# Performance work log

Hardware: AMD Instinct MI355X
Metric: run time of the kernel (lower is better)

The kernel has to match this reference:

```python
import jax, jax.numpy as jnp
import numpy as np

B_SZ, L, D, N = 4, 2048, 768, 16


def setup_inputs() -> dict:
    key = jax.random.key(0)
    ks = jax.random.split(key, 8)
    x = jax.random.normal(ks[0], (B_SZ, L, D), dtype=jnp.float32)
    # A_log initialized as log(arange(1..N)) repeated over d, as in the module
    A_log = jnp.log(jnp.broadcast_to(jnp.arange(1, N + 1, dtype=jnp.float32), (D, N)))
    # s_b_c: Linear(D, 2N)
    W_bc = jax.random.normal(ks[1], (2 * N, D), dtype=jnp.float32) / jnp.sqrt(D)
    b_bc = jnp.zeros((2 * N,), dtype=jnp.float32)
    # s_1: Linear(D, 1)
    W_1 = jax.random.normal(ks[2], (1, D), dtype=jnp.float32) / jnp.sqrt(D)
    b_1 = jnp.zeros((1,), dtype=jnp.float32)
    # s_delta: Linear(1, D)
    W_d = jax.random.normal(ks[3], (D, 1), dtype=jnp.float32)
    b_d = jnp.zeros((D,), dtype=jnp.float32)
    return {"x": x, "A_log": A_log, "W_bc": W_bc, "b_bc": b_bc,
            "W_1": W_1, "b_1": b_1, "W_d": W_d, "b_d": b_d}


def reference(x, A_log, W_bc, b_bc, W_1, b_1, W_d, b_d):
    b, l, d = x.shape
    n = A_log.shape[1]
    A = -jnp.exp(A_log)                                   # (d, n)
    BandC = x @ W_bc.T + b_bc                             # (b, l, 2n)
    Bm, Cm = BandC[..., :n], BandC[..., n:]               # (b, l, n) each
    # delta = softplus(s_delta(s_1(x)))  -> (b, l, d)
    s1 = x @ W_1.T + b_1                                  # (b, l, 1)
    delta = jax.nn.softplus(s1 @ W_d.T + b_d)             # (b, l, d)
    deltaA = jnp.exp(jnp.einsum('bld,dn->bldn', delta, A))        # (b, l, d, n)
    deltaB_u = jnp.einsum('bld,bln,bld->bldn', delta, Bm, x)      # (b, l, d, n)

    # sequential selective-scan over time with lax.scan
    dA_t = jnp.moveaxis(deltaA, 1, 0)      # (l, b, d, n)
    dBu_t = jnp.moveaxis(deltaB_u, 1, 0)   # (l, b, d, n)
    C_t = jnp.moveaxis(Cm, 1, 0)           # (l, b, n)

    def step(h, inp):
        dA_i, dBu_i, c_i = inp
        h = dA_i * h + dBu_i               # (b, d, n)
        y = jnp.einsum('bdn,bn->bd', h, c_i)
        return h, y

    h0 = jnp.zeros((b, d, n), dtype=x.dtype)
    _, ys = jax.lax.scan(step, h0, (dA_t, dBu_t, C_t))
    return jnp.moveaxis(ys, 0, 1)          # (b, l, d)
```

## Files before the change

kernel.cpp:

```cpp
#include <hip/hip_runtime.h>

#define L_SEQ 2048
#define D_DIM 768
#define N_ST 16
#define NB 4
#define NJ 33
#define NROWS (NB * L_SEQ)
#define PROJ_ELEMS (NROWS * NJ)

#define DSPLIT 8
#define DSEG (D_DIM / DSPLIT)
#define DK 32
#define NCHUNK (DSEG / DK)
#define RB 128
#define XST 132
#define WST 64

__device__ __forceinline__ float fast_exp2(float x) {
#if __has_builtin(__builtin_amdgcn_exp2f)
  return __builtin_amdgcn_exp2f(x);
#else
  return __expf(x * 0.69314718055994531f);
#endif
}

__device__ __forceinline__ float softplus_f(float v) {
  float e = fast_exp2(v * 1.44269504088896f);
  float l = __log2f(1.0f + e) * 0.69314718055994531f;
  return (v > 15.0f) ? v : l;
}

__device__ __forceinline__ void pow_tree(float e1, float pw[N_ST]) {
  pw[0] = e1;
  pw[1] = pw[0] * pw[0];
  pw[2] = pw[1] * pw[0];
  pw[3] = pw[1] * pw[1];
  pw[4] = pw[3] * pw[0];
  pw[5] = pw[3] * pw[1];
  pw[6] = pw[3] * pw[2];
  pw[7] = pw[3] * pw[3];
  pw[8] = pw[7] * pw[0];
  pw[9] = pw[7] * pw[1];
  pw[10] = pw[7] * pw[2];
  pw[11] = pw[7] * pw[3];
  pw[12] = pw[7] * pw[4];
  pw[13] = pw[7] * pw[5];
  pw[14] = pw[7] * pw[6];
  pw[15] = pw[7] * pw[7];
}

__global__ __launch_bounds__(256) void k_proj_gemm(
    const float* __restrict__ x, const float* __restrict__ W_bc,
    const float* __restrict__ W_1, float* __restrict__ PBC) {
  __shared__ float xs_t[DK * XST];
  __shared__ float ws_t[DK * WST];

  const int ds  = blockIdx.x % DSPLIT;
  const int rb0 = (blockIdx.x / DSPLIT) * RB;
  const int dbase = ds * DSEG;
  const int tid = threadIdx.x;

  const int rg = tid & 31;
  const int jg = tid >> 5;

  float acc[4][5];
#pragma unroll
  for (int i = 0; i < 4; ++i)
#pragma unroll
    for (int k = 0; k < 5; ++k) acc[i][k] = 0.0f;

  const int lrow = tid >> 1;
  const int lhalf = (tid & 1) * 16;
  const float* xg_row = x + (size_t)(rb0 + lrow) * D_DIM + dbase + lhalf;

  for (int ch = 0; ch < NCHUNK; ++ch) {
    const int dc = dbase + ch * DK;
    float4 xv[4];
#pragma unroll
    for (int q = 0; q < 4; ++q)
      xv[q] = *(const float4*)(xg_row + ch * DK + q * 4);
    float wv[8];
    int widx[8];
#pragma unroll
    for (int u = 0; u < 8; ++u) {
      int idx = tid + u * 256;
      int dk = idx >> 6, slot = idx & 63;
      int wjg = slot >> 3, wk = slot & 7;
      int j = wjg + 8 * wk;
      float v = 0.0f;
      if (wk < 5) {
        if (j < 32)       v = W_bc[(size_t)j * D_DIM + dc + dk];
        else if (j == 32) v = W_1[dc + dk];
      }
      wv[u] = v; widx[u] = dk * WST + slot;
    }
    __syncthreads();
#pragma unroll
    for (int q = 0; q < 4; ++q) {
      xs_t[(lhalf + q * 4 + 0) * XST + lrow] = xv[q].x;
      xs_t[(lhalf + q * 4 + 1) * XST + lrow] = xv[q].y;
      xs_t[(lhalf + q * 4 + 2) * XST + lrow] = xv[q].z;
      xs_t[(lhalf + q * 4 + 3) * XST + lrow] = xv[q].w;
    }
#pragma unroll
    for (int u = 0; u < 8; ++u) ws_t[widx[u]] = wv[u];
    __syncthreads();
#pragma unroll 8
    for (int dk = 0; dk < DK; ++dk) {
      float4 xr = *(const float4*)&xs_t[dk * XST + rg * 4];
      float4 wr = *(const float4*)&ws_t[dk * WST + jg * 8];
      float w4  = ws_t[dk * WST + jg * 8 + 4];
      float xa[4] = {xr.x, xr.y, xr.z, xr.w};
      float wa[5] = {wr.x, wr.y, wr.z, wr.w, w4};
#pragma unroll
      for (int i = 0; i < 4; ++i)
#pragma unroll
        for (int k = 0; k < 5; ++k)
          acc[i][k] = fmaf(xa[i], wa[k], acc[i][k]);
    }
  }

  float* pb = PBC + (size_t)ds * PROJ_ELEMS;
#pragma unroll
  for (int i = 0; i < 4; ++i) {
    int row = rb0 + rg * 4 + i;
#pragma unroll
    for (int k = 0; k < 5; ++k) {
      int j = jg + 8 * k;
      if (k < 4 || jg == 0) pb[(size_t)row * NJ + j] = acc[i][k];
    }
  }
}

__global__ __launch_bounds__(256) void k_proj_reduce(
    const float* __restrict__ PBC, const float* __restrict__ b_bc,
    const float* __restrict__ b_1, float* __restrict__ BC33) {
  const int idx = blockIdx.x * 256 + threadIdx.x;
  const int j = idx % NJ;
  float s = 0.0f;
#pragma unroll
  for (int k = 0; k < DSPLIT; ++k) s += PBC[(size_t)k * PROJ_ELEMS + idx];
  s += (j < 32) ? b_bc[j] : b_1[0];
  BC33[idx] = s;
}

template <int LC>
__global__ __launch_bounds__(256) void k_scan1(
    const float* __restrict__ x, const float* __restrict__ A_log,
    const float* __restrict__ W_d, const float* __restrict__ b_d,
    const float* __restrict__ BC33, float* __restrict__ DS,
    float* __restrict__ H, int NC) {
  const int cb = blockIdx.x % 3;
  const int c  = (blockIdx.x / 3) % NC;
  const int b  = blockIdx.x / (3 * NC);
  const int d  = cb * 256 + threadIdx.x;

  const float wd = W_d[d], bd = b_d[d];
  float Aln[N_ST];
  {
    const float4* al4 = (const float4*)(A_log + (size_t)d * N_ST);
#pragma unroll
    for (int q = 0; q < 4; ++q) {
      float4 v = al4[q];
      Aln[4*q+0] = -__expf(v.x) * 1.44269504088896f;
      Aln[4*q+1] = -__expf(v.y) * 1.44269504088896f;
      Aln[4*q+2] = -__expf(v.z) * 1.44269504088896f;
      Aln[4*q+3] = -__expf(v.w) * 1.44269504088896f;
    }
  }

  bool geom = true;
#pragma unroll
  for (int n = 1; n < N_ST; ++n) {
    float ref = (float)(n + 1) * Aln[0];
    geom = geom && (fabsf(Aln[n] - ref) <= 1e-4f * fabsf(ref) + 1e-12f);
  }
  const float a0 = Aln[0];

  float h[N_ST];
#pragma unroll
  for (int n = 0; n < N_ST; ++n) h[n] = 0.0f;
  float dsum = 0.0f;

  const int l0 = c * LC;
  const float* bc = BC33 + (size_t)(b * L_SEQ + l0) * NJ;
  const float* xp = x + (size_t)(b * L_SEQ + l0) * D_DIM + d;

  if (geom) {
#pragma unroll 8
    for (int l = 0; l < LC; ++l) {
      float s1 = bc[l * NJ + 32];
      float delta = softplus_f(fmaf(s1, wd, bd));
      float xv = xp[(size_t)l * D_DIM];
      float f = delta * xv;
      dsum += delta;
      float pw[N_ST];
      pow_tree(fast_exp2(a0 * delta), pw);
#pragma unroll
      for (int n = 0; n < N_ST; ++n)
        h[n] = fmaf(pw[n], h[n], f * bc[l * NJ + n]);
    }
  } else {
#pragma unroll 4
    for (int l = 0; l < LC; ++l) {
      float s1 = bc[l * NJ + 32];
      float delta = softplus_f(fmaf(s1, wd, bd));
      float xv = xp[(size_t)l * D_DIM];
      float f = delta * xv;
      dsum += delta;
#pragma unroll
      for (int n = 0; n < N_ST; ++n) {
        float dA = fast_exp2(delta * Aln[n]);
        h[n] = fmaf(dA, h[n], f * bc[l * NJ + n]);
      }
    }
  }

  DS[((size_t)b * NC + c) * D_DIM + d] = dsum;
  size_t base = ((size_t)(b * NC + c) * D_DIM + d) * N_ST;
  float4* H4 = (float4*)(H + base);
#pragma unroll
  for (int q = 0; q < 4; ++q)
    H4[q] = make_float4(h[4*q], h[4*q+1], h[4*q+2], h[4*q+3]);
}

__global__ __launch_bounds__(256) void k_combine(
    const float* __restrict__ A_log, const float* __restrict__ DS,
    float* __restrict__ H, int NC) {
  const int b  = blockIdx.x / 48;
  const int tl = (blockIdx.x % 48) * 256 + threadIdx.x;
  const int d = tl >> 4, n = tl & 15;
  const float Aln = -__expf(A_log[d * N_ST + n]) * 1.44269504088896f;

  const float* dsp = DS + (size_t)b * NC * D_DIM + d;
  float* Hp = H + (size_t)b * NC * (D_DIM * N_ST) + tl;

  float h = 0.0f;
  float ds_c = dsp[0];
  float hold = Hp[0];
#pragma unroll 8
  for (int c = 0; c < NC; ++c) {
    float ds_n = 0.0f, hold_n = 0.0f;
    if (c + 1 < NC) {
      ds_n   = dsp[(size_t)(c + 1) * D_DIM];
      hold_n = Hp[(size_t)(c + 1) * (D_DIM * N_ST)];
    }
    float p = fast_exp2(Aln * ds_c);
    Hp[(size_t)c * (D_DIM * N_ST)] = h;
    h = fmaf(p, h, hold);
    ds_c = ds_n; hold = hold_n;
  }
}

template <int LC>
__global__ __launch_bounds__(256) void k_scan2(
    const float* __restrict__ x, const float* __restrict__ A_log,
    const float* __restrict__ W_d, const float* __restrict__ b_d,
    const float* __restrict__ BC33, const float* __restrict__ HIN,
    float* __restrict__ out, int NC) {
  const int cb = blockIdx.x % 3;
  const int c  = (blockIdx.x / 3) % NC;
  const int b  = blockIdx.x / (3 * NC);
  const int d  = cb * 256 + threadIdx.x;

  const float wd = W_d[d], bd = b_d[d];
  float Aln[N_ST];
  {
    const float4* al4 = (const float4*)(A_log + (size_t)d * N_ST);
#pragma unroll
    for (int q = 0; q < 4; ++q) {
      float4 v = al4[q];
      Aln[4*q+0] = -__expf(v.x) * 1.44269504088896f;
      Aln[4*q+1] = -__expf(v.y) * 1.44269504088896f;
      Aln[4*q+2] = -__expf(v.z) * 1.44269504088896f;
      Aln[4*q+3] = -__expf(v.w) * 1.44269504088896f;
    }
  }

  bool geom = true;
#pragma unroll
  for (int n = 1; n < N_ST; ++n) {
    float ref = (float)(n + 1) * Aln[0];
    geom = geom && (fabsf(Aln[n] - ref) <= 1e-4f * fabsf(ref) + 1e-12f);
  }
  const float a0 = Aln[0];

  float h[N_ST];
  size_t base = ((size_t)(b * NC + c) * D_DIM + d) * N_ST;
  const float4* HIN4 = (const float4*)(HIN + base);
#pragma unroll
  for (int q = 0; q < 4; ++q) {
    float4 v = HIN4[q];
    h[4*q] = v.x; h[4*q+1] = v.y; h[4*q+2] = v.z; h[4*q+3] = v.w;
  }

  const int l0 = c * LC;
  const float* bc = BC33 + (size_t)(b * L_SEQ + l0) * NJ;
  const float* xp = x + (size_t)(b * L_SEQ + l0) * D_DIM + d;
  float* op = out + (size_t)(b * L_SEQ + l0) * D_DIM + d;

  if (geom) {
#pragma unroll 8
    for (int l = 0; l < LC; ++l) {
      float s1 = bc[l * NJ + 32];
      float delta = softplus_f(fmaf(s1, wd, bd));
      float xv = xp[(size_t)l * D_DIM];
      float f = delta * xv;
      float pw[N_ST];
      pow_tree(fast_exp2(a0 * delta), pw);
      float y = 0.0f;
#pragma unroll
      for (int n = 0; n < N_ST; ++n) {
        h[n] = fmaf(pw[n], h[n], f * bc[l * NJ + n]);
        y = fmaf(h[n], bc[l * NJ + 16 + n], y);
      }
      op[(size_t)l * D_DIM] = y;
    }
  } else {
#pragma unroll 4
    for (int l = 0; l < LC; ++l) {
      float s1 = bc[l * NJ + 32];
      float delta = softplus_f(fmaf(s1, wd, bd));
      float xv = xp[(size_t)l * D_DIM];
      float f = delta * xv;
      float y = 0.0f;
#pragma unroll
      for (int n = 0; n < N_ST; ++n) {
        float dA = fast_exp2(delta * Aln[n]);
        h[n] = fmaf(dA, h[n], f * bc[l * NJ + n]);
        y = fmaf(h[n], bc[l * NJ + 16 + n], y);
      }
      op[(size_t)l * D_DIM] = y;
    }
  }
}

extern "C" void kernel_launch(void* const* d_in, const int* in_sizes, int n_in,
                              void* d_out, int out_size, void* d_ws, size_t ws_size,
                              hipStream_t stream) {
  const float* x     = (const float*)d_in[0];
  const float* A_log = (const float*)d_in[1];
  const float* W_bc  = (const float*)d_in[2];
  const float* b_bc  = (const float*)d_in[3];
  const float* W_1   = (const float*)d_in[4];
  const float* b_1   = (const float*)d_in[5];
  const float* W_d   = (const float*)d_in[6];
  const float* b_d   = (const float*)d_in[7];
  float* out = (float*)d_out;
  float* ws  = (float*)d_ws;

  int NC = 8;
  const int cands[4] = {64, 32, 16, 8};
  for (int i = 0; i < 4; ++i) {
    size_t need = (9ull * PROJ_ELEMS + (3072ull + 49152ull) * cands[i]) * 4ull;
    if (ws_size >= need) { NC = cands[i]; break; }
  }

  float* BC33 = ws;
  float* PBC  = ws + PROJ_ELEMS;
  float* DSb  = PBC + (size_t)DSPLIT * PROJ_ELEMS;
  float* H    = DSb + (size_t)3072 * NC;

  k_proj_gemm<<<(NROWS / RB) * DSPLIT, 256, 0, stream>>>(x, W_bc, W_1, PBC);
  k_proj_reduce<<<PROJ_ELEMS / 256, 256, 0, stream>>>(PBC, b_bc, b_1, BC33);

  const int gs = 3 * NB * NC;
  switch (NC) {
    case 64:
      k_scan1<32><<<gs, 256, 0, stream>>>(x, A_log, W_d, b_d, BC33, DSb, H, NC);
      k_combine<<<192, 256, 0, stream>>>(A_log, DSb, H, NC);
      k_scan2<32><<<gs, 256, 0, stream>>>(x, A_log, W_d, b_d, BC33, H, out, NC);
      break;
    case 32:
      k_scan1<64><<<gs, 256, 0, stream>>>(x, A_log, W_d, b_d, BC33, DSb, H, NC);
      k_combine<<<192, 256, 0, stream>>>(A_log, DSb, H, NC);
      k_scan2<64><<<gs, 256, 0, stream>>>(x, A_log, W_d, b_d, BC33, H, out, NC);
      break;
    case 16:
      k_scan1<128><<<gs, 256, 0, stream>>>(x, A_log, W_d, b_d, BC33, DSb, H, NC);
      k_combine<<<192, 256, 0, stream>>>(A_log, DSb, H, NC);
      k_scan2<128><<<gs, 256, 0, stream>>>(x, A_log, W_d, b_d, BC33, H, out, NC);
      break;
    default:
      k_scan1<256><<<gs, 256, 0, stream>>>(x, A_log, W_d, b_d, BC33, DSb, H, NC);
      k_combine<<<192, 256, 0, stream>>>(A_log, DSb, H, NC);
      k_scan2<256><<<gs, 256, 0, stream>>>(x, A_log, W_d, b_d, BC33, H, out, NC);
      break;
  }
}
```

Before: 170.4 us.

## Fuse chunked scan phases into one cooperative kernel with cached local outputs

Replaces the three scan kernels (chunk scan, cross-chunk combine, rescan) with one cooperative kernel that uses grid syncs between phases. The first pass keeps the zero-initial-state outputs in LDS. The second pass no longer reruns the recurrence; it adds a correction term built from the carried-in state, the cumulative delta decay and C. Packed float2 math is used for the geometric power tree. This removes two launches and the redundant recurrence and x reads, at the cost of 32KB LDS per block, grid-wide barriers and a co-residency requirement for 768 blocks, with a fallback path if the cooperative launch fails.

New measurement: 359.5 us. 111% more time.

```diff
diff --git a/kernel.cpp b/kernel.cpp
--- a/kernel.cpp
+++ b/kernel.cpp
@@ -1,4 +1,7 @@
 #include <hip/hip_runtime.h>
+#include <hip/hip_cooperative_groups.h>
+
+namespace cg = cooperative_groups;
 
 #define L_SEQ 2048
 #define D_DIM 768
@@ -7,6 +10,7 @@
 #define NJ 33
 #define NROWS (NB * L_SEQ)
 #define PROJ_ELEMS (NROWS * NJ)
+#define DN (D_DIM * N_ST)
 
 #define DSPLIT 8
 #define DSEG (D_DIM / DSPLIT)
@@ -16,6 +20,8 @@
 #define XST 132
 #define WST 64
 
+typedef float v2f __attribute__((ext_vector_type(2)));
+
 __device__ __forceinline__ float fast_exp2(float x) {
 #if __has_builtin(__builtin_amdgcn_exp2f)
   return __builtin_amdgcn_exp2f(x);
@@ -30,23 +36,26 @@
   return (v > 15.0f) ? v : l;
 }
 
+__device__ __forceinline__ void pow_tree2(float e1, v2f pw2[8]) {
+  float e2s = e1 * e1;
+  float e4s = e2s * e2s;
+  float e8s = e4s * e4s;
+  v2f s2 = {e2s, e2s}, s4 = {e4s, e4s}, s8 = {e8s, e8s};
+  pw2[0] = (v2f){e1, e2s};
+  pw2[1] = pw2[0] * s2;
+  pw2[2] = pw2[0] * s4;
+  pw2[3] = pw2[1] * s4;
+  pw2[4] = pw2[0] * s8;
+  pw2[5] = pw2[1] * s8;
+  pw2[6] = pw2[2] * s8;
+  pw2[7] = pw2[3] * s8;
+}
+
 __device__ __forceinline__ void pow_tree(float e1, float pw[N_ST]) {
-  pw[0] = e1;
-  pw[1] = pw[0] * pw[0];
-  pw[2] = pw[1] * pw[0];
-  pw[3] = pw[1] * pw[1];
-  pw[4] = pw[3] * pw[0];
-  pw[5] = pw[3] * pw[1];
-  pw[6] = pw[3] * pw[2];
-  pw[7] = pw[3] * pw[3];
-  pw[8] = pw[7] * pw[0];
-  pw[9] = pw[7] * pw[1];
-  pw[10] = pw[7] * pw[2];
-  pw[11] = pw[7] * pw[3];
-  pw[12] = pw[7] * pw[4];
-  pw[13] = pw[7] * pw[5];
-  pw[14] = pw[7] * pw[6];
-  pw[15] = pw[7] * pw[7];
+  pw[0] = e1;  pw[1] = pw[0]*pw[0];  pw[2] = pw[1]*pw[0];  pw[3] = pw[1]*pw[1];
+  pw[4] = pw[3]*pw[0]; pw[5] = pw[3]*pw[1]; pw[6] = pw[3]*pw[2]; pw[7] = pw[3]*pw[3];
+  pw[8] = pw[7]*pw[0]; pw[9] = pw[7]*pw[1]; pw[10]= pw[7]*pw[2]; pw[11]= pw[7]*pw[3];
+  pw[12]= pw[7]*pw[4]; pw[13]= pw[7]*pw[5]; pw[14]= pw[7]*pw[6]; pw[15]= pw[7]*pw[7];
 }
 
 __global__ __launch_bounds__(256) void k_proj_gemm(
@@ -59,7 +68,6 @@
   const int rb0 = (blockIdx.x / DSPLIT) * RB;
   const int dbase = ds * DSEG;
   const int tid = threadIdx.x;
-
   const int rg = tid & 31;
   const int jg = tid >> 5;
 
@@ -142,6 +150,197 @@
   for (int k = 0; k < DSPLIT; ++k) s += PBC[(size_t)k * PROJ_ELEMS + idx];
   s += (j < 32) ? b_bc[j] : b_1[0];
   BC33[idx] = s;
+}
+
+template <int LC>
+__global__ __launch_bounds__(256) void k_scan_coop(
+    const float* __restrict__ x, const float* __restrict__ A_log,
+    const float* __restrict__ W_d, const float* __restrict__ b_d,
+    const float* __restrict__ BC33, float* __restrict__ DS,
+    float* __restrict__ H, float* __restrict__ out) {
+  constexpr int NC = L_SEQ / LC;
+  __shared__ float ylds[LC * 256];
+  const int tid = threadIdx.x;
+  const int bid = blockIdx.x;
+  const int cb = bid % 3;
+  const int c  = (bid / 3) % NC;
+  const int b  = bid / (3 * NC);
+  const int d  = cb * 256 + tid;
+
+  const float wd = W_d[d], bd = b_d[d];
+  float Aln[N_ST];
+  {
+    const float4* al4 = (const float4*)(A_log + (size_t)d * N_ST);
+#pragma unroll
+    for (int q = 0; q < 4; ++q) {
+      float4 v = al4[q];
+      Aln[4*q+0] = -__expf(v.x) * 1.44269504088896f;
+      Aln[4*q+1] = -__expf(v.y) * 1.44269504088896f;
+      Aln[4*q+2] = -__expf(v.z) * 1.44269504088896f;
+      Aln[4*q+3] = -__expf(v.w) * 1.44269504088896f;
+    }
+  }
+  bool geom = true;
+#pragma unroll
+  for (int n = 1; n < N_ST; ++n) {
+    float ref = (float)(n + 1) * Aln[0];
+    geom = geom && (fabsf(Aln[n] - ref) <= 1e-4f * fabsf(ref) + 1e-12f);
+  }
+  const float a0 = Aln[0];
+
+  const int l0 = c * LC;
+  const float* bc = BC33 + (size_t)(b * L_SEQ + l0) * NJ;
+  const float* xp = x + (size_t)(b * L_SEQ + l0) * D_DIM + d;
+
+  v2f h2[8];
+#pragma unroll
+  for (int k = 0; k < 8; ++k) h2[k] = (v2f){0.0f, 0.0f};
+  float dsum = 0.0f;
+
+  if (geom) {
+#pragma unroll 8
+    for (int l = 0; l < LC; ++l) {
+      float s1 = bc[l * NJ + 32];
+      float delta = softplus_f(fmaf(s1, wd, bd));
+      float xv = xp[(size_t)l * D_DIM];
+      float f = delta * xv;
+      dsum += delta;
+      v2f pw2[8];
+      pow_tree2(fast_exp2(a0 * delta), pw2);
+      v2f f2 = {f, f};
+      v2f y2 = {0.0f, 0.0f};
+#pragma unroll
+      for (int k = 0; k < 8; ++k) {
+        v2f B2 = {bc[l * NJ + 2*k], bc[l * NJ + 2*k + 1]};
+        v2f C2 = {bc[l * NJ + 16 + 2*k], bc[l * NJ + 16 + 2*k + 1]};
+        h2[k] = pw2[k] * h2[k] + f2 * B2;
+        y2 = y2 + h2[k] * C2;
+      }
+      ylds[l * 256 + tid] = y2.x + y2.y;
+    }
+  } else {
+#pragma unroll 4
+    for (int l = 0; l < LC; ++l) {
+      float s1 = bc[l * NJ + 32];
+      float delta = softplus_f(fmaf(s1, wd, bd));
+      float xv = xp[(size_t)l * D_DIM];
+      float f = delta * xv;
+      dsum += delta;
+      float y = 0.0f;
+#pragma unroll
+      for (int k = 0; k < 8; ++k) {
+        float dA0 = fast_exp2(delta * Aln[2*k]);
+        float dA1 = fast_exp2(delta * Aln[2*k+1]);
+        h2[k].x = fmaf(dA0, h2[k].x, f * bc[l * NJ + 2*k]);
+        h2[k].y = fmaf(dA1, h2[k].y, f * bc[l * NJ + 2*k + 1]);
+        y = fmaf(h2[k].x, bc[l * NJ + 16 + 2*k], y);
+        y = fmaf(h2[k].y, bc[l * NJ + 16 + 2*k + 1], y);
+      }
+      ylds[l * 256 + tid] = y;
+    }
+  }
+
+  DS[((size_t)b * NC + c) * D_DIM + d] = dsum;
+  {
+    size_t base = ((size_t)(b * NC + c) * D_DIM + d) * N_ST;
+    float4* H4 = (float4*)(H + base);
+#pragma unroll
+    for (int q = 0; q < 4; ++q)
+      H4[q] = make_float4(h2[2*q].x, h2[2*q].y, h2[2*q+1].x, h2[2*q+1].y);
+  }
+
+  cg::this_grid().sync();
+
+  if (bid < 192) {
+    const int bb = bid / 48;
+    const int tl = (bid % 48) * 256 + tid;
+    const int dd = tl >> 4, nn = tl & 15;
+    const float Aln1 = -__expf(A_log[dd * N_ST + nn]) * 1.44269504088896f;
+    const float* dsp = DS + (size_t)bb * NC * D_DIM + dd;
+    float* Hp = H + (size_t)bb * NC * DN + tl;
+
+    float h = 0.0f;
+    float pds[8], ph[8];
+#pragma unroll
+    for (int k = 0; k < 8; ++k) {
+      pds[k] = dsp[(size_t)k * D_DIM];
+      ph[k]  = Hp[(size_t)k * DN];
+    }
+    for (int g = 0; g < NC; g += 8) {
+      float nds[8], nh[8];
+      if (g + 8 < NC) {
+#pragma unroll
+        for (int k = 0; k < 8; ++k) {
+          nds[k] = dsp[(size_t)(g + 8 + k) * D_DIM];
+          nh[k]  = Hp[(size_t)(g + 8 + k) * DN];
+        }
+      }
+#pragma unroll
+      for (int k = 0; k < 8; ++k) {
+        float p = fast_exp2(Aln1 * pds[k]);
+        Hp[(size_t)(g + k) * DN] = h;
+        h = fmaf(p, h, ph[k]);
+      }
+#pragma unroll
+      for (int k = 0; k < 8; ++k) { pds[k] = nds[k]; ph[k] = nh[k]; }
+    }
+  }
+
+  cg::this_grid().sync();
+
+  float* op = out + (size_t)(b * L_SEQ + l0) * D_DIM + d;
+  if (c == 0) {
+#pragma unroll 8
+    for (int l = 0; l < LC; ++l)
+      op[(size_t)l * D_DIM] = ylds[l * 256 + tid];
+    return;
+  }
+
+  v2f hin2[8];
+  {
+    size_t base = ((size_t)(b * NC + c) * D_DIM + d) * N_ST;
+    const float4* HIN4 = (const float4*)(H + base);
+#pragma unroll
+    for (int q = 0; q < 4; ++q) {
+      float4 v = HIN4[q];
+      hin2[2*q]   = (v2f){v.x, v.y};
+      hin2[2*q+1] = (v2f){v.z, v.w};
+    }
+  }
+
+  if (geom) {
+    float S = 0.0f;
+#pragma unroll 8
+    for (int l = 0; l < LC; ++l) {
+      float s1 = bc[l * NJ + 32];
+      float delta = softplus_f(fmaf(s1, wd, bd));
+      S += delta;
+      v2f pw2[8];
+      pow_tree2(fast_exp2(a0 * S), pw2);
+      v2f acc = {0.0f, 0.0f};
+#pragma unroll
+      for (int k = 0; k < 8; ++k) {
+        v2f C2 = {bc[l * NJ + 16 + 2*k], bc[l * NJ + 16 + 2*k + 1]};
+        acc = acc + pw2[k] * (hin2[k] * C2);
+      }
+      op[(size_t)l * D_DIM] = ylds[l * 256 + tid] + acc.x + acc.y;
+    }
+  } else {
+    float S = 0.0f;
+#pragma unroll 4
+    for (int l = 0; l < LC; ++l) {
+      float s1 = bc[l * NJ + 32];
+      float delta = softplus_f(fmaf(s1, wd, bd));
+      S += delta;
+      float corr = 0.0f;
+#pragma unroll
+      for (int k = 0; k < 8; ++k) {
+        corr = fmaf(fast_exp2(Aln[2*k]   * S) * hin2[k].x, bc[l * NJ + 16 + 2*k],     corr);
+        corr = fmaf(fast_exp2(Aln[2*k+1] * S) * hin2[k].y, bc[l * NJ + 16 + 2*k + 1], corr);
+      }
+      op[(size_t)l * D_DIM] = ylds[l * 256 + tid] + corr;
+    }
+  }
 }
 
 template <int LC>
@@ -154,21 +353,11 @@
   const int c  = (blockIdx.x / 3) % NC;
   const int b  = blockIdx.x / (3 * NC);
   const int d  = cb * 256 + threadIdx.x;
-
   const float wd = W_d[d], bd = b_d[d];
   float Aln[N_ST];
-  {
-    const float4* al4 = (const float4*)(A_log + (size_t)d * N_ST);
-#pragma unroll
-    for (int q = 0; q < 4; ++q) {
-      float4 v = al4[q];
-      Aln[4*q+0] = -__expf(v.x) * 1.44269504088896f;
-      Aln[4*q+1] = -__expf(v.y) * 1.44269504088896f;
-      Aln[4*q+2] = -__expf(v.z) * 1.44269504088896f;
-      Aln[4*q+3] = -__expf(v.w) * 1.44269504088896f;
-    }
-  }
-
+#pragma unroll
+  for (int n = 0; n < N_ST; ++n)
+    Aln[n] = -__expf(A_log[d * N_ST + n]) * 1.44269504088896f;
   bool geom = true;
 #pragma unroll
   for (int n = 1; n < N_ST; ++n) {
@@ -176,23 +365,19 @@
     geom = geom && (fabsf(Aln[n] - ref) <= 1e-4f * fabsf(ref) + 1e-12f);
   }
   const float a0 = Aln[0];
-
   float h[N_ST];
 #pragma unroll
   for (int n = 0; n < N_ST; ++n) h[n] = 0.0f;
   float dsum = 0.0f;
-
   const int l0 = c * LC;
   const float* bc = BC33 + (size_t)(b * L_SEQ + l0) * NJ;
   const float* xp = x + (size_t)(b * L_SEQ + l0) * D_DIM + d;
-
   if (geom) {
 #pragma unroll 8
     for (int l = 0; l < LC; ++l) {
       float s1 = bc[l * NJ + 32];
       float delta = softplus_f(fmaf(s1, wd, bd));
-      float xv = xp[(size_t)l * D_DIM];
-      float f = delta * xv;
+      float f = delta * xp[(size_t)l * D_DIM];
       dsum += delta;
       float pw[N_ST];
       pow_tree(fast_exp2(a0 * delta), pw);
@@ -205,17 +390,13 @@
     for (int l = 0; l < LC; ++l) {
       float s1 = bc[l * NJ + 32];
       float delta = softplus_f(fmaf(s1, wd, bd));
-      float xv = xp[(size_t)l * D_DIM];
-      float f = delta * xv;
+      float f = delta * xp[(size_t)l * D_DIM];
       dsum += delta;
 #pragma unroll
-      for (int n = 0; n < N_ST; ++n) {
-        float dA = fast_exp2(delta * Aln[n]);
-        h[n] = fmaf(dA, h[n], f * bc[l * NJ + n]);
-      }
-    }
-  }
-
+      for (int n = 0; n < N_ST; ++n)
+        h[n] = fmaf(fast_exp2(delta * Aln[n]), h[n], f * bc[l * NJ + n]);
+    }
+  }
   DS[((size_t)b * NC + c) * D_DIM + d] = dsum;
   size_t base = ((size_t)(b * NC + c) * D_DIM + d) * N_ST;
   float4* H4 = (float4*)(H + base);
@@ -231,10 +412,8 @@
   const int tl = (blockIdx.x % 48) * 256 + threadIdx.x;
   const int d = tl >> 4, n = tl & 15;
   const float Aln = -__expf(A_log[d * N_ST + n]) * 1.44269504088896f;
-
   const float* dsp = DS + (size_t)b * NC * D_DIM + d;
-  float* Hp = H + (size_t)b * NC * (D_DIM * N_ST) + tl;
-
+  float* Hp = H + (size_t)b * NC * DN + tl;
   float h = 0.0f;
   float ds_c = dsp[0];
   float hold = Hp[0];
@@ -243,10 +422,10 @@
     float ds_n = 0.0f, hold_n = 0.0f;
     if (c + 1 < NC) {
       ds_n   = dsp[(size_t)(c + 1) * D_DIM];
-      hold_n = Hp[(size_t)(c + 1) * (D_DIM * N_ST)];
+      hold_n = Hp[(size_t)(c + 1) * DN];
     }
     float p = fast_exp2(Aln * ds_c);
-    Hp[(size_t)c * (D_DIM * N_ST)] = h;
+    Hp[(size_t)c * DN] = h;
     h = fmaf(p, h, hold);
     ds_c = ds_n; hold = hold_n;
   }
@@ -262,21 +441,11 @@
   const int c  = (blockIdx.x / 3) % NC;
   const int b  = blockIdx.x / (3 * NC);
   const int d  = cb * 256 + threadIdx.x;
-
   const float wd = W_d[d], bd = b_d[d];
   float Aln[N_ST];
-  {
-    const float4* al4 = (const float4*)(A_log + (size_t)d * N_ST);
-#pragma unroll
-    for (int q = 0; q < 4; ++q) {
-      float4 v = al4[q];
-      Aln[4*q+0] = -__expf(v.x) * 1.44269504088896f;
-      Aln[4*q+1] = -__expf(v.y) * 1.44269504088896f;
-      Aln[4*q+2] = -__expf(v.z) * 1.44269504088896f;
-      Aln[4*q+3] = -__expf(v.w) * 1.44269504088896f;
-    }
-  }
-
+#pragma unroll
+  for (int n = 0; n < N_ST; ++n)
+    Aln[n] = -__expf(A_log[d * N_ST + n]) * 1.44269504088896f;
   bool geom = true;
 #pragma unroll
   for (int n = 1; n < N_ST; ++n) {
@@ -284,7 +453,6 @@
     geom = geom && (fabsf(Aln[n] - ref) <= 1e-4f * fabsf(ref) + 1e-12f);
   }
   const float a0 = Aln[0];
-
   float h[N_ST];
   size_t base = ((size_t)(b * NC + c) * D_DIM + d) * N_ST;
   const float4* HIN4 = (const float4*)(HIN + base);
@@ -293,19 +461,16 @@
     float4 v = HIN4[q];
     h[4*q] = v.x; h[4*q+1] = v.y; h[4*q+2] = v.z; h[4*q+3] = v.w;
   }
-
   const int l0 = c * LC;
   const float* bc = BC33 + (size_t)(b * L_SEQ + l0) * NJ;
   const float* xp = x + (size_t)(b * L_SEQ + l0) * D_DIM + d;
   float* op = out + (size_t)(b * L_SEQ + l0) * D_DIM + d;
-
   if (geom) {
 #pragma unroll 8
     for (int l = 0; l < LC; ++l) {
       float s1 = bc[l * NJ + 32];
       float delta = softplus_f(fmaf(s1, wd, bd));
-      float xv = xp[(size_t)l * D_DIM];
-      float f = delta * xv;
+      float f = delta * xp[(size_t)l * D_DIM];
       float pw[N_ST];
       pow_tree(fast_exp2(a0 * delta), pw);
       float y = 0.0f;
@@ -321,13 +486,11 @@
     for (int l = 0; l < LC; ++l) {
       float s1 = bc[l * NJ + 32];
       float delta = softplus_f(fmaf(s1, wd, bd));
-      float xv = xp[(size_t)l * D_DIM];
-      float f = delta * xv;
+      float f = delta * xp[(size_t)l * D_DIM];
       float y = 0.0f;
 #pragma unroll
       for (int n = 0; n < N_ST; ++n) {
-        float dA = fast_exp2(delta * Aln[n]);
-        h[n] = fmaf(dA, h[n], f * bc[l * NJ + n]);
+        h[n] = fmaf(fast_exp2(delta * Aln[n]), h[n], f * bc[l * NJ + n]);
         y = fmaf(h[n], bc[l * NJ + 16 + n], y);
       }
       op[(size_t)l * D_DIM] = y;
@@ -349,11 +512,10 @@
   float* out = (float*)d_out;
   float* ws  = (float*)d_ws;
 
-  int NC = 8;
-  const int cands[4] = {64, 32, 16, 8};
-  for (int i = 0; i < 4; ++i) {
-    size_t need = (9ull * PROJ_ELEMS + (3072ull + 49152ull) * cands[i]) * 4ull;
-    if (ws_size >= need) { NC = cands[i]; break; }
+  int NC = 64;
+  {
+    size_t need = (9ull * PROJ_ELEMS + (3072ull + 49152ull) * 64) * 4ull;
+    if (ws_size < need) NC = 32;
   }
 
   float* BC33 = ws;
@@ -365,26 +527,30 @@
   k_proj_reduce<<<PROJ_ELEMS / 256, 256, 0, stream>>>(PBC, b_bc, b_1, BC33);
 
   const int gs = 3 * NB * NC;
-  switch (NC) {
-    case 64:
+  const float* xa = x; const float* ala = A_log;
+  const float* wda = W_d; const float* bda = b_d;
+  const float* bca = BC33; float* dsa = DSb; float* ha = H; float* oa = out;
+  void* args[] = {(void*)&xa, (void*)&ala, (void*)&wda, (void*)&bda,
+                  (void*)&bca, (void*)&dsa, (void*)&ha, (void*)&oa};
+
+  hipError_t ce;
+  if (NC == 64) {
+    ce = hipLaunchCooperativeKernel(reinterpret_cast<void*>(&k_scan_coop<32>),
+                                    dim3(gs), dim3(256), args, 0, stream);
+  } else {
+    ce = hipLaunchCooperativeKernel(reinterpret_cast<void*>(&k_scan_coop<64>),
+                                    dim3(gs), dim3(256), args, 0, stream);
+  }
+  if (ce != hipSuccess) {
+    (void)hipGetLastError();
+    if (NC == 64) {
       k_scan1<32><<<gs, 256, 0, stream>>>(x, A_log, W_d, b_d, BC33, DSb, H, NC);
       k_combine<<<192, 256, 0, stream>>>(A_log, DSb, H, NC);
       k_scan2<32><<<gs, 256, 0, stream>>>(x, A_log, W_d, b_d, BC33, H, out, NC);
-      break;
-    case 32:
+    } else {
       k_scan1<64><<<gs, 256, 0, stream>>>(x, A_log, W_d, b_d, BC33, DSb, H, NC);
       k_combine<<<192, 256, 0, stream>>>(A_log, DSb, H, NC);
       k_scan2<64><<<gs, 256, 0, stream>>>(x, A_log, W_d, b_d, BC33, H, out, NC);
-      break;
-    case 16:
-      k_scan1<128><<<gs, 256, 0, stream>>>(x, A_log, W_d, b_d, BC33, DSb, H, NC);
-      k_combine<<<192, 256, 0, stream>>>(A_log, DSb, H, NC);
-      k_scan2<128><<<gs, 256, 0, stream>>>(x, A_log, W_d, b_d, BC33, H, out, NC);
-      break;
-    default:
-      k_scan1<256><<<gs, 256, 0, stream>>>(x, A_log, W_d, b_d, BC33, DSb, H, NC);
-      k_combine<<<192, 256, 0, stream>>>(A_log, DSb, H, NC);
-      k_scan2<256><<<gs, 256, 0, stream>>>(x, A_log, W_d, b_d, BC33, H, out, NC);
-      break;
-  }
-}
+    }
+  }
+}
```

## Pad BC rows to 48 floats, vectorize scan with packed float2 math, batch combine loads

Applied to the files above, without the earlier changes.

The projection reduce now writes B, C and s1 into rows padded to 48 floats, so the scan kernels can read B and C with aligned float4 loads instead of scalar loads at stride 33. The state recurrence and the output dot product are rewritten over two-wide float vectors, aiming at packed FP32 instructions, and the power tree is built the same way. The chunk-combine kernel loads eight chunks at a time to overlap memory latency. The padding enlarges the BC buffer, and the workspace sizing now falls back only to 32 chunks.

After: 151.9 us. 1.12x faster.

```diff
diff --git a/kernel.cpp b/kernel.cpp
--- a/kernel.cpp
+++ b/kernel.cpp
@@ -5,8 +5,10 @@
 #define N_ST 16
 #define NB 4
 #define NJ 33
+#define BCS 48
 #define NROWS (NB * L_SEQ)
 #define PROJ_ELEMS (NROWS * NJ)
+#define DN (D_DIM * N_ST)
 
 #define DSPLIT 8
 #define DSEG (D_DIM / DSPLIT)
@@ -16,6 +18,8 @@
 #define XST 132
 #define WST 64
 
+typedef float v2f __attribute__((ext_vector_type(2)));
+
 __device__ __forceinline__ float fast_exp2(float x) {
 #if __has_builtin(__builtin_amdgcn_exp2f)
   return __builtin_amdgcn_exp2f(x);
@@ -30,23 +34,19 @@
   return (v > 15.0f) ? v : l;
 }
 
-__device__ __forceinline__ void pow_tree(float e1, float pw[N_ST]) {
-  pw[0] = e1;
-  pw[1] = pw[0] * pw[0];
-  pw[2] = pw[1] * pw[0];
-  pw[3] = pw[1] * pw[1];
-  pw[4] = pw[3] * pw[0];
-  pw[5] = pw[3] * pw[1];
-  pw[6] = pw[3] * pw[2];
-  pw[7] = pw[3] * pw[3];
-  pw[8] = pw[7] * pw[0];
-  pw[9] = pw[7] * pw[1];
-  pw[10] = pw[7] * pw[2];
-  pw[11] = pw[7] * pw[3];
-  pw[12] = pw[7] * pw[4];
-  pw[13] = pw[7] * pw[5];
-  pw[14] = pw[7] * pw[6];
-  pw[15] = pw[7] * pw[7];
+__device__ __forceinline__ void pow_tree2(float e1, v2f pw2[8]) {
+  float e2s = e1 * e1;
+  float e4s = e2s * e2s;
+  float e8s = e4s * e4s;
+  v2f s2 = {e2s, e2s}, s4 = {e4s, e4s}, s8 = {e8s, e8s};
+  pw2[0] = (v2f){e1, e2s};
+  pw2[1] = pw2[0] * s2;
+  pw2[2] = pw2[0] * s4;
+  pw2[3] = pw2[1] * s4;
+  pw2[4] = pw2[0] * s8;
+  pw2[5] = pw2[1] * s8;
+  pw2[6] = pw2[2] * s8;
+  pw2[7] = pw2[3] * s8;
 }
 
 __global__ __launch_bounds__(256) void k_proj_gemm(
@@ -59,7 +59,6 @@
   const int rb0 = (blockIdx.x / DSPLIT) * RB;
   const int dbase = ds * DSEG;
   const int tid = threadIdx.x;
-
   const int rg = tid & 31;
   const int jg = tid >> 5;
 
@@ -134,21 +133,22 @@
 
 __global__ __launch_bounds__(256) void k_proj_reduce(
     const float* __restrict__ PBC, const float* __restrict__ b_bc,
-    const float* __restrict__ b_1, float* __restrict__ BC33) {
+    const float* __restrict__ b_1, float* __restrict__ BC48) {
   const int idx = blockIdx.x * 256 + threadIdx.x;
-  const int j = idx % NJ;
+  const int row = idx / NJ;
+  const int j = idx - row * NJ;
   float s = 0.0f;
 #pragma unroll
   for (int k = 0; k < DSPLIT; ++k) s += PBC[(size_t)k * PROJ_ELEMS + idx];
   s += (j < 32) ? b_bc[j] : b_1[0];
-  BC33[idx] = s;
+  BC48[(size_t)row * BCS + j] = s;
 }
 
 template <int LC>
 __global__ __launch_bounds__(256) void k_scan1(
     const float* __restrict__ x, const float* __restrict__ A_log,
     const float* __restrict__ W_d, const float* __restrict__ b_d,
-    const float* __restrict__ BC33, float* __restrict__ DS,
+    const float* __restrict__ BC48, float* __restrict__ DS,
     float* __restrict__ H, int NC) {
   const int cb = blockIdx.x % 3;
   const int c  = (blockIdx.x / 3) % NC;
@@ -168,7 +168,6 @@
       Aln[4*q+3] = -__expf(v.w) * 1.44269504088896f;
     }
   }
-
   bool geom = true;
 #pragma unroll
   for (int n = 1; n < N_ST; ++n) {
@@ -177,41 +176,52 @@
   }
   const float a0 = Aln[0];
 
-  float h[N_ST];
-#pragma unroll
-  for (int n = 0; n < N_ST; ++n) h[n] = 0.0f;
+  v2f h2[8];
+#pragma unroll
+  for (int k = 0; k < 8; ++k) h2[k] = (v2f){0.0f, 0.0f};
   float dsum = 0.0f;
 
   const int l0 = c * LC;
-  const float* bc = BC33 + (size_t)(b * L_SEQ + l0) * NJ;
+  const float* bc = BC48 + (size_t)(b * L_SEQ + l0) * BCS;
   const float* xp = x + (size_t)(b * L_SEQ + l0) * D_DIM + d;
 
   if (geom) {
 #pragma unroll 8
     for (int l = 0; l < LC; ++l) {
-      float s1 = bc[l * NJ + 32];
+      const float* r = bc + l * BCS;
+      float4 B0 = *(const float4*)(r + 0);
+      float4 B1 = *(const float4*)(r + 4);
+      float4 B2 = *(const float4*)(r + 8);
+      float4 B3 = *(const float4*)(r + 12);
+      float s1 = r[32];
       float delta = softplus_f(fmaf(s1, wd, bd));
       float xv = xp[(size_t)l * D_DIM];
       float f = delta * xv;
       dsum += delta;
-      float pw[N_ST];
-      pow_tree(fast_exp2(a0 * delta), pw);
-#pragma unroll
-      for (int n = 0; n < N_ST; ++n)
-        h[n] = fmaf(pw[n], h[n], f * bc[l * NJ + n]);
+      v2f pw2[8];
+      pow_tree2(fast_exp2(a0 * delta), pw2);
+      v2f f2 = {f, f};
+      h2[0] = pw2[0] * h2[0] + f2 * (v2f){B0.x, B0.y};
+      h2[1] = pw2[1] * h2[1] + f2 * (v2f){B0.z, B0.w};
+      h2[2] = pw2[2] * h2[2] + f2 * (v2f){B1.x, B1.y};
+      h2[3] = pw2[3] * h2[3] + f2 * (v2f){B1.z, B1.w};
+      h2[4] = pw2[4] * h2[4] + f2 * (v2f){B2.x, B2.y};
+      h2[5] = pw2[5] * h2[5] + f2 * (v2f){B2.z, B2.w};
+      h2[6] = pw2[6] * h2[6] + f2 * (v2f){B3.x, B3.y};
+      h2[7] = pw2[7] * h2[7] + f2 * (v2f){B3.z, B3.w};
     }
   } else {
 #pragma unroll 4
     for (int l = 0; l < LC; ++l) {
-      float s1 = bc[l * NJ + 32];
+      const float* r = bc + l * BCS;
+      float s1 = r[32];
       float delta = softplus_f(fmaf(s1, wd, bd));
-      float xv = xp[(size_t)l * D_DIM];
-      float f = delta * xv;
+      float f = delta * xp[(size_t)l * D_DIM];
       dsum += delta;
 #pragma unroll
-      for (int n = 0; n < N_ST; ++n) {
-        float dA = fast_exp2(delta * Aln[n]);
-        h[n] = fmaf(dA, h[n], f * bc[l * NJ + n]);
+      for (int k = 0; k < 8; ++k) {
+        h2[k].x = fmaf(fast_exp2(delta * Aln[2*k]),   h2[k].x, f * r[2*k]);
+        h2[k].y = fmaf(fast_exp2(delta * Aln[2*k+1]), h2[k].y, f * r[2*k+1]);
       }
     }
   }
@@ -221,7 +231,7 @@
   float4* H4 = (float4*)(H + base);
 #pragma unroll
   for (int q = 0; q < 4; ++q)
-    H4[q] = make_float4(h[4*q], h[4*q+1], h[4*q+2], h[4*q+3]);
+    H4[q] = make_float4(h2[2*q].x, h2[2*q].y, h2[2*q+1].x, h2[2*q+1].y);
 }
 
 __global__ __launch_bounds__(256) void k_combine(
@@ -230,25 +240,34 @@
   const int b  = blockIdx.x / 48;
   const int tl = (blockIdx.x % 48) * 256 + threadIdx.x;
   const int d = tl >> 4, n = tl & 15;
-  const float Aln = -__expf(A_log[d * N_ST + n]) * 1.44269504088896f;
-
+  const float Aln1 = -__expf(A_log[d * N_ST + n]) * 1.44269504088896f;
   const float* dsp = DS + (size_t)b * NC * D_DIM + d;
-  float* Hp = H + (size_t)b * NC * (D_DIM * N_ST) + tl;
+  float* Hp = H + (size_t)b * NC * DN + tl;
 
   float h = 0.0f;
-  float ds_c = dsp[0];
-  float hold = Hp[0];
-#pragma unroll 8
-  for (int c = 0; c < NC; ++c) {
-    float ds_n = 0.0f, hold_n = 0.0f;
-    if (c + 1 < NC) {
-      ds_n   = dsp[(size_t)(c + 1) * D_DIM];
-      hold_n = Hp[(size_t)(c + 1) * (D_DIM * N_ST)];
-    }
-    float p = fast_exp2(Aln * ds_c);
-    Hp[(size_t)c * (D_DIM * N_ST)] = h;
-    h = fmaf(p, h, hold);
-    ds_c = ds_n; hold = hold_n;
+  float pds[8], ph[8];
+#pragma unroll
+  for (int k = 0; k < 8; ++k) {
+    pds[k] = dsp[(size_t)k * D_DIM];
+    ph[k]  = Hp[(size_t)k * DN];
+  }
+  for (int g = 0; g < NC; g += 8) {
+    float nds[8], nh[8];
+    if (g + 8 < NC) {
+#pragma unroll
+      for (int k = 0; k < 8; ++k) {
+        nds[k] = dsp[(size_t)(g + 8 + k) * D_DIM];
+        nh[k]  = Hp[(size_t)(g + 8 + k) * DN];
+      }
+    }
+#pragma unroll
+    for (int k = 0; k < 8; ++k) {
+      float p = fast_exp2(Aln1 * pds[k]);
+      Hp[(size_t)(g + k) * DN] = h;
+      h = fmaf(p, h, ph[k]);
+    }
+#pragma unroll
+    for (int k = 0; k < 8; ++k) { pds[k] = nds[k]; ph[k] = nh[k]; }
   }
 }
 
@@ -256,7 +275,7 @@
 __global__ __launch_bounds__(256) void k_scan2(
     const float* __restrict__ x, const float* __restrict__ A_log,
     const float* __restrict__ W_d, const float* __restrict__ b_d,
-    const float* __restrict__ BC33, const float* __restrict__ HIN,
+    const float* __restrict__ BC48, const float* __restrict__ HIN,
     float* __restrict__ out, int NC) {
   const int cb = blockIdx.x % 3;
   const int c  = (blockIdx.x / 3) % NC;
@@ -276,7 +295,6 @@
       Aln[4*q+3] = -__expf(v.w) * 1.44269504088896f;
     }
   }
-
   bool geom = true;
 #pragma unroll
   for (int n = 1; n < N_ST; ++n) {
@@ -285,50 +303,67 @@
   }
   const float a0 = Aln[0];
 
-  float h[N_ST];
-  size_t base = ((size_t)(b * NC + c) * D_DIM + d) * N_ST;
-  const float4* HIN4 = (const float4*)(HIN + base);
-#pragma unroll
-  for (int q = 0; q < 4; ++q) {
-    float4 v = HIN4[q];
-    h[4*q] = v.x; h[4*q+1] = v.y; h[4*q+2] = v.z; h[4*q+3] = v.w;
+  v2f h2[8];
+  {
+    size_t base = ((size_t)(b * NC + c) * D_DIM + d) * N_ST;
+    const float4* HIN4 = (const float4*)(HIN + base);
+#pragma unroll
+    for (int q = 0; q < 4; ++q) {
+      float4 v = HIN4[q];
+      h2[2*q]   = (v2f){v.x, v.y};
+      h2[2*q+1] = (v2f){v.z, v.w};
+    }
   }
 
   const int l0 = c * LC;
-  const float* bc = BC33 + (size_t)(b * L_SEQ + l0) * NJ;
+  const float* bc = BC48 + (size_t)(b * L_SEQ + l0) * BCS;
   const float* xp = x + (size_t)(b * L_SEQ + l0) * D_DIM + d;
   float* op = out + (size_t)(b * L_SEQ + l0) * D_DIM + d;
 
   if (geom) {
 #pragma unroll 8
     for (int l = 0; l < LC; ++l) {
-      float s1 = bc[l * NJ + 32];
+      const float* r = bc + l * BCS;
+      float4 B0 = *(const float4*)(r + 0);
+      float4 B1 = *(const float4*)(r + 4);
+      float4 B2 = *(const float4*)(r + 8);
+      float4 B3 = *(const float4*)(r + 12);
+      float4 C0 = *(const float4*)(r + 16);
+      float4 C1 = *(const float4*)(r + 20);
+      float4 C2 = *(const float4*)(r + 24);
+      float4 C3 = *(const float4*)(r + 28);
+      float s1 = r[32];
       float delta = softplus_f(fmaf(s1, wd, bd));
       float xv = xp[(size_t)l * D_DIM];
       float f = delta * xv;
-      float pw[N_ST];
-      pow_tree(fast_exp2(a0 * delta), pw);
-      float y = 0.0f;
-#pragma unroll
-      for (int n = 0; n < N_ST; ++n) {
-        h[n] = fmaf(pw[n], h[n], f * bc[l * NJ + n]);
-        y = fmaf(h[n], bc[l * NJ + 16 + n], y);
-      }
-      op[(size_t)l * D_DIM] = y;
+      v2f pw2[8];
+      pow_tree2(fast_exp2(a0 * delta), pw2);
+      v2f f2 = {f, f};
+      v2f y2 = {0.0f, 0.0f};
+      h2[0] = pw2[0] * h2[0] + f2 * (v2f){B0.x, B0.y};  y2 += h2[0] * (v2f){C0.x, C0.y};
+      h2[1] = pw2[1] * h2[1] + f2 * (v2f){B0.z, B0.w};  y2 += h2[1] * (v2f){C0.z, C0.w};
+      h2[2] = pw2[2] * h2[2] + f2 * (v2f){B1.x, B1.y};  y2 += h2[2] * (v2f){C1.x, C1.y};
+      h2[3] = pw2[3] * h2[3] + f2 * (v2f){B1.z, B1.w};  y2 += h2[3] * (v2f){C1.z, C1.w};
+      h2[4] = pw2[4] * h2[4] + f2 * (v2f){B2.x, B2.y};  y2 += h2[4] * (v2f){C2.x, C2.y};
+      h2[5] = pw2[5] * h2[5] + f2 * (v2f){B2.z, B2.w};  y2 += h2[5] * (v2f){C2.z, C2.w};
+      h2[6] = pw2[6] * h2[6] + f2 * (v2f){B3.x, B3.y};  y2 += h2[6] * (v2f){C3.x, C3.y};
+      h2[7] = pw2[7] * h2[7] + f2 * (v2f){B3.z, B3.w};  y2 += h2[7] * (v2f){C3.z, C3.w};
+      op[(size_t)l * D_DIM] = y2.x + y2.y;
     }
   } else {
 #pragma unroll 4
     for (int l = 0; l < LC; ++l) {
-      float s1 = bc[l * NJ + 32];
+      const float* r = bc + l * BCS;
+      float s1 = r[32];
       float delta = softplus_f(fmaf(s1, wd, bd));
-      float xv = xp[(size_t)l * D_DIM];
-      float f = delta * xv;
+      float f = delta * xp[(size_t)l * D_DIM];
       float y = 0.0f;
 #pragma unroll
-      for (int n = 0; n < N_ST; ++n) {
-        float dA = fast_exp2(delta * Aln[n]);
-        h[n] = fmaf(dA, h[n], f * bc[l * NJ + n]);
-        y = fmaf(h[n], bc[l * NJ + 16 + n], y);
+      for (int k = 0; k < 8; ++k) {
+        h2[k].x = fmaf(fast_exp2(delta * Aln[2*k]),   h2[k].x, f * r[2*k]);
+        h2[k].y = fmaf(fast_exp2(delta * Aln[2*k+1]), h2[k].y, f * r[2*k+1]);
+        y = fmaf(h2[k].x, r[16 + 2*k], y);
+        y = fmaf(h2[k].y, r[16 + 2*k + 1], y);
       }
       op[(size_t)l * D_DIM] = y;
     }
@@ -349,42 +384,29 @@
   float* out = (float*)d_out;
   float* ws  = (float*)d_ws;
 
-  int NC = 8;
-  const int cands[4] = {64, 32, 16, 8};
-  for (int i = 0; i < 4; ++i) {
-    size_t need = (9ull * PROJ_ELEMS + (3072ull + 49152ull) * cands[i]) * 4ull;
-    if (ws_size >= need) { NC = cands[i]; break; }
-  }
-
-  float* BC33 = ws;
-  float* PBC  = ws + PROJ_ELEMS;
+  int NC = 64;
+  {
+    size_t need = ((size_t)NROWS * BCS + 8ull * PROJ_ELEMS +
+                   (3072ull + 49152ull) * 64) * 4ull;
+    if (ws_size < need) NC = 32;
+  }
+
+  float* BC48 = ws;
+  float* PBC  = ws + (size_t)NROWS * BCS;
   float* DSb  = PBC + (size_t)DSPLIT * PROJ_ELEMS;
   float* H    = DSb + (size_t)3072 * NC;
 
   k_proj_gemm<<<(NROWS / RB) * DSPLIT, 256, 0, stream>>>(x, W_bc, W_1, PBC);
-  k_proj_reduce<<<PROJ_ELEMS / 256, 256, 0, stream>>>(PBC, b_bc, b_1, BC33);
+  k_proj_reduce<<<(PROJ_ELEMS + 255) / 256, 256, 0, stream>>>(PBC, b_bc, b_1, BC48);
 
   const int gs = 3 * NB * NC;
-  switch (NC) {
-    case 64:
-      k_scan1<32><<<gs, 256, 0, stream>>>(x, A_log, W_d, b_d, BC33, DSb, H, NC);
-      k_combine<<<192, 256, 0, stream>>>(A_log, DSb, H, NC);
-      k_scan2<32><<<gs, 256, 0, stream>>>(x, A_log, W_d, b_d, BC33, H, out, NC);
-      break;
-    case 32:
-      k_scan1<64><<<gs, 256, 0, stream>>>(x, A_log, W_d, b_d, BC33, DSb, H, NC);
-      k_combine<<<192, 256, 0, stream>>>(A_log, DSb, H, NC);
-      k_scan2<64><<<gs, 256, 0, stream>>>(x, A_log, W_d, b_d, BC33, H, out, NC);
-      break;
-    case 16:
-      k_scan1<128><<<gs, 256, 0, stream>>>(x, A_log, W_d, b_d, BC33, DSb, H, NC);
-      k_combine<<<192, 256, 0, stream>>>(A_log, DSb, H, NC);
-      k_scan2<128><<<gs, 256, 0, stream>>>(x, A_log, W_d, b_d, BC33, H, out, NC);
-      break;
-    default:
-      k_scan1<256><<<gs, 256, 0, stream>>>(x, A_log, W_d, b_d, BC33, DSb, H, NC);
-      k_combine<<<192, 256, 0, stream>>>(A_log, DSb, H, NC);
-      k_scan2<256><<<gs, 256, 0, stream>>>(x, A_log, W_d, b_d, BC33, H, out, NC);
-      break;
-  }
-}
+  if (NC == 64) {
+    k_scan1<32><<<gs, 256, 0, stream>>>(x, A_log, W_d, b_d, BC48, DSb, H, NC);
+    k_combine<<<192, 256, 0, stream>>>(A_log, DSb, H, NC);
+    k_scan2<32><<<gs, 256, 0, stream>>>(x, A_log, W_d, b_d, BC48, H, out, NC);
+  } else {
+    k_scan1<64><<<gs, 256, 0, stream>>>(x, A_log, W_d, b_d, BC48, DSb, H, NC);
+    k_combine<<<192, 256, 0, stream>>>(A_log, DSb, H, NC);
+    k_scan2<64><<<gs, 256, 0, stream>>>(x, A_log, W_d, b_d, BC48, H, out, NC);
+  }
+}
```
